# Optimization experiments

Measured on AMD Instinct MI355X. Metric: run time of the kernel, lower is better.

## Reference

```python
import jax, jax.numpy as jnp
import numpy as np

LN_EPS = 1e-5
FACTOR = 4

def layer_norm(x, w, b):
    mu = jnp.mean(x, axis=-1, keepdims=True)
    var = jnp.mean((x - mu) ** 2, axis=-1, keepdims=True)
    return (x - mu) * jax.lax.rsqrt(var + LN_EPS) * w + b

def setup_inputs() -> dict:
    key = jax.random.key(0)
    k1, k2, k3 = jax.random.split(key, 3)
    B, Sq, Skv, D = 4, 2048, 8192, 1024
    return {
        "query": jax.random.normal(k1, (B, Sq, D), dtype=jnp.float32),
        "key": jax.random.normal(k2, (B, Skv, D), dtype=jnp.float32),
        "value": jax.random.normal(k3, (B, Skv, D), dtype=jnp.float32),
        "ln_weight": jnp.ones((D,), dtype=jnp.float32),
        "ln_bias": jnp.zeros((D,), dtype=jnp.float32),
    }

def attention_downsampling(q, k, v, factor):
    # q: [B, S//f, D], k/v: [B, S, D]
    B, S, D = k.shape
    k_win = k.reshape(B, S // factor, factor, D)
    weights = jnp.einsum('bsd,bsfd->bsf', q, k_win).reshape(B, S)  # no softmax
    attn = weights[:, :, None] * v                                  # [B, S, D]
    attn = attn.reshape(B, S // factor, factor, D).sum(axis=2)      # [B, S//f, D]
    return attn

def reference(query, key, value, ln_weight, ln_bias):
    # pre-norm (post_norm=False): residual + attention over normed q/k/v
    qn = layer_norm(query, ln_weight, ln_bias)
    kn = layer_norm(key, ln_weight, ln_bias)
    vn = layer_norm(value, ln_weight, ln_bias)
    return query + attention_downsampling(qn, kn, vn, FACTOR)
```

## Files before the change

kernel.cpp:

```cpp
#include <hip/hip_runtime.h>


constexpr int D     = 1024;
constexpr int BLOCK = 256;
constexpr int NW    = BLOCK / 64;
constexpr float EPS = 1e-5f;

#define GLOBAL_AS const __attribute__((address_space(1))) void*
#define LDS_AS __attribute__((address_space(3))) void*

template<int CTRL>
__device__ __forceinline__ float dpp_add(float x) {
    int xi = __builtin_bit_cast(int, x);
    int yi = __builtin_amdgcn_update_dpp(0, xi, CTRL, 0xF, 0xF, true);
    return x + __builtin_bit_cast(float, yi);
}

__device__ __forceinline__ float wave_sum(float x) {
    x = dpp_add<0x111>(x);
    x = dpp_add<0x112>(x);
    x = dpp_add<0x114>(x);
    x = dpp_add<0x118>(x);
    x = dpp_add<0x142>(x);
    x = dpp_add<0x143>(x);
    return __builtin_bit_cast(float, __builtin_amdgcn_readlane(__builtin_bit_cast(int, x), 63));
}

template <int N>
__device__ __forceinline__ void block_reduce(float* vals, float* s_buf,
                                             int lane, int wid) {
#pragma unroll
    for (int i = 0; i < N; i++) {
        float x = wave_sum(vals[i]);
        if (lane == 0) s_buf[wid * N + i] = x;
    }
    __syncthreads();
#pragma unroll
    for (int i = 0; i < N; i++) {
        float t = 0.f;
#pragma unroll
        for (int w = 0; w < NW; w++) t += s_buf[w * N + i];
        vals[i] = t;
    }
    __syncthreads();
}

__global__ __launch_bounds__(BLOCK) void attn_ds_kernel(
    const float* __restrict__ q,
    const float* __restrict__ k,
    const float* __restrict__ v,
    const float* __restrict__ lw,
    const float* __restrict__ lb,
    float* __restrict__ out)
{
    __shared__ float kv_lds[8 * D];
    __shared__ float s_buf[NW * 18];

    const long row  = blockIdx.x;
    const int  tid  = threadIdx.x;
    const int  lane = tid & 63;
    const int  wid  = tid >> 6;
    const int  d0   = tid * 4;

    const float4 qv = *(const float4*)(q + row * D + d0);
    const float4 wv = *(const float4*)(lw + d0);
    const float4 bv = *(const float4*)(lb + d0);

    const float* kbase = k + row * (4L * D);
    const float* vbase = v + row * (4L * D);
#pragma unroll
    for (int i = 0; i < 8; i++) {
        const int c = wid + i * NW;
        const float* src = (c < 16 ? kbase : vbase) + (long)(c & 15) * 256 + lane * 4;
        float* dst = kv_lds + c * 256;
        __builtin_amdgcn_global_load_lds((GLOBAL_AS)src, (LDS_AS)dst, 16, 0, 0);
    }

    __syncthreads();

    float red[18];
    red[0] = qv.x + qv.y + qv.z + qv.w;
    red[1] = qv.x * qv.x + qv.y * qv.y + qv.z * qv.z + qv.w * qv.w;
    float4 kv4[4], vv4[4];
#pragma unroll
    for (int f = 0; f < 4; f++) {
        kv4[f] = *(const float4*)(kv_lds + f * D + d0);
        vv4[f] = *(const float4*)(kv_lds + (4 + f) * D + d0);
        red[2 + 2 * f]  = kv4[f].x + kv4[f].y + kv4[f].z + kv4[f].w;
        red[3 + 2 * f]  = kv4[f].x * kv4[f].x + kv4[f].y * kv4[f].y
                        + kv4[f].z * kv4[f].z + kv4[f].w * kv4[f].w;
        red[10 + 2 * f] = vv4[f].x + vv4[f].y + vv4[f].z + vv4[f].w;
        red[11 + 2 * f] = vv4[f].x * vv4[f].x + vv4[f].y * vv4[f].y
                        + vv4[f].z * vv4[f].z + vv4[f].w * vv4[f].w;
    }
    block_reduce<18>(red, s_buf, lane, wid);

    const float invD = 1.0f / (float)D;
    const float mu_q = red[0] * invD;
    const float rs_q = rsqrtf(fmaf(-mu_q, mu_q, red[1] * invD) + EPS);
    float mu_k[4], rs_k[4], mu_v[4], rs_v[4];
#pragma unroll
    for (int f = 0; f < 4; f++) {
        mu_k[f] = red[2 + 2 * f] * invD;
        rs_k[f] = rsqrtf(fmaf(-mu_k[f], mu_k[f], red[3 + 2 * f] * invD) + EPS);
        mu_v[f] = red[10 + 2 * f] * invD;
        rs_v[f] = rsqrtf(fmaf(-mu_v[f], mu_v[f], red[11 + 2 * f] * invD) + EPS);
    }

    float4 qn;
    qn.x = fmaf((qv.x - mu_q) * rs_q, wv.x, bv.x);
    qn.y = fmaf((qv.y - mu_q) * rs_q, wv.y, bv.y);
    qn.z = fmaf((qv.z - mu_q) * rs_q, wv.z, bv.z);
    qn.w = fmaf((qv.w - mu_q) * rs_q, wv.w, bv.w);
    float dp[4];
#pragma unroll
    for (int f = 0; f < 4; f++) {
        float4 kn;
        kn.x = fmaf((kv4[f].x - mu_k[f]) * rs_k[f], wv.x, bv.x);
        kn.y = fmaf((kv4[f].y - mu_k[f]) * rs_k[f], wv.y, bv.y);
        kn.z = fmaf((kv4[f].z - mu_k[f]) * rs_k[f], wv.z, bv.z);
        kn.w = fmaf((kv4[f].w - mu_k[f]) * rs_k[f], wv.w, bv.w);
        dp[f] = qn.x * kn.x + qn.y * kn.y + qn.z * kn.z + qn.w * kn.w;
    }
    block_reduce<4>(dp, s_buf, lane, wid);

    float4 acc = qv;
#pragma unroll
    for (int f = 0; f < 4; f++) {
        const float av = rs_v[f], cv = -mu_v[f] * rs_v[f], dpf = dp[f];
#define ACCO(m) { \
        float t  = fmaf(av, vv4[f].m, cv); \
        float vn = fmaf(t, wv.m, bv.m); \
        acc.m = fmaf(dpf, vn, acc.m); }
        ACCO(x) ACCO(y) ACCO(z) ACCO(w)
#undef ACCO
    }
    *(float4*)(out + row * D + d0) = acc;
}

extern "C" void kernel_launch(void* const* d_in, const int* in_sizes, int n_in,
                              void* d_out, int out_size, void* d_ws, size_t ws_size,
                              hipStream_t stream) {
    const float* q  = (const float*)d_in[0];
    const float* k  = (const float*)d_in[1];
    const float* v  = (const float*)d_in[2];
    const float* lw = (const float*)d_in[3];
    const float* lb = (const float*)d_in[4];
    float* out = (float*)d_out;

    const int rows = in_sizes[0] / D;
    attn_ds_kernel<<<dim3(rows), dim3(BLOCK), 0, stream>>>(q, k, v, lw, lb, out);
}
```

Baseline: 310.5 us.

## Process sixteen rows per block with double-buffered async LDS staging

Each block now handles sixteen consecutive rows, staging q, k and v for the next row into a second LDS buffer via global_load_lds while the current row is computed. Hand-placed vmcnt waits and raw barriers replace __syncthreads, and the trailing barrier of the last reduction is dropped. This is meant to overlap memory latency with compute and cut per-block launch overhead. In exchange it uses 72KB of LDS per block and launches far fewer blocks, which limits resident blocks per CU and may reduce the number of memory requests in flight.

```diff
diff --git a/kernel.cpp b/kernel.cpp
--- a/kernel.cpp
+++ b/kernel.cpp
@@ -4,6 +4,7 @@
 constexpr int D     = 1024;
 constexpr int BLOCK = 256;
 constexpr int NW    = BLOCK / 64;
+constexpr int NR    = 16;
 constexpr float EPS = 1e-5f;
 
 #define GLOBAL_AS const __attribute__((address_space(1))) void*
@@ -26,7 +27,13 @@
     return __builtin_bit_cast(float, __builtin_amdgcn_readlane(__builtin_bit_cast(int, x), 63));
 }
 
-template <int N>
+__device__ __forceinline__ void bar_lds() {
+    asm volatile("s_waitcnt lgkmcnt(0)" ::: "memory");
+    __builtin_amdgcn_s_barrier();
+    asm volatile("" ::: "memory");
+}
+
+template <int N, bool TRAIL>
 __device__ __forceinline__ void block_reduce(float* vals, float* s_buf,
                                              int lane, int wid) {
 #pragma unroll
@@ -34,7 +41,7 @@
         float x = wave_sum(vals[i]);
         if (lane == 0) s_buf[wid * N + i] = x;
     }
-    __syncthreads();
+    bar_lds();
 #pragma unroll
     for (int i = 0; i < N; i++) {
         float t = 0.f;
@@ -42,50 +49,43 @@
         for (int w = 0; w < NW; w++) t += s_buf[w * N + i];
         vals[i] = t;
     }
-    __syncthreads();
+    if (TRAIL) bar_lds();
 }
 
-__global__ __launch_bounds__(BLOCK) void attn_ds_kernel(
-    const float* __restrict__ q,
-    const float* __restrict__ k,
-    const float* __restrict__ v,
-    const float* __restrict__ lw,
-    const float* __restrict__ lb,
-    float* __restrict__ out)
-{
-    __shared__ float kv_lds[8 * D];
-    __shared__ float s_buf[NW * 18];
+__device__ __forceinline__ void stage_row(const float* __restrict__ q,
+                                          const float* __restrict__ k,
+                                          const float* __restrict__ v,
+                                          long row, float* buf, int wid, int lane) {
+    const int lo = lane * 4;
+    __builtin_amdgcn_global_load_lds((GLOBAL_AS)(q + row * D + wid * 256 + lo),
+                                     (LDS_AS)(buf + wid * 256), 16, 0, 0);
+    const float* kb = k + row * (4L * D) + wid * 256 + lo;
+    const float* vb = v + row * (4L * D) + wid * 256 + lo;
+    float* dk = buf + 1024 + wid * 256;
+    float* dv = buf + 5120 + wid * 256;
+#pragma unroll
+    for (int i = 0; i < 4; i++)
+        __builtin_amdgcn_global_load_lds((GLOBAL_AS)(kb + i * 1024),
+                                         (LDS_AS)(dk + i * 1024), 16, 0, 0);
+#pragma unroll
+    for (int i = 0; i < 4; i++)
+        __builtin_amdgcn_global_load_lds((GLOBAL_AS)(vb + i * 1024),
+                                         (LDS_AS)(dv + i * 1024), 16, 0, 0);
+}
 
-    const long row  = blockIdx.x;
-    const int  tid  = threadIdx.x;
-    const int  lane = tid & 63;
-    const int  wid  = tid >> 6;
-    const int  d0   = tid * 4;
-
-    const float4 qv = *(const float4*)(q + row * D + d0);
-    const float4 wv = *(const float4*)(lw + d0);
-    const float4 bv = *(const float4*)(lb + d0);
-
-    const float* kbase = k + row * (4L * D);
-    const float* vbase = v + row * (4L * D);
-#pragma unroll
-    for (int i = 0; i < 8; i++) {
-        const int c = wid + i * NW;
-        const float* src = (c < 16 ? kbase : vbase) + (long)(c & 15) * 256 + lane * 4;
-        float* dst = kv_lds + c * 256;
-        __builtin_amdgcn_global_load_lds((GLOBAL_AS)src, (LDS_AS)dst, 16, 0, 0);
-    }
-
-    __syncthreads();
-
+__device__ __forceinline__ void compute_row(const float* buf, float* s_buf,
+                                            const float4 wv, const float4 bv,
+                                            float* __restrict__ outp,
+                                            int lane, int wid, int d0) {
+    const float4 qv = *(const float4*)(buf + d0);
     float red[18];
     red[0] = qv.x + qv.y + qv.z + qv.w;
     red[1] = qv.x * qv.x + qv.y * qv.y + qv.z * qv.z + qv.w * qv.w;
     float4 kv4[4], vv4[4];
 #pragma unroll
     for (int f = 0; f < 4; f++) {
-        kv4[f] = *(const float4*)(kv_lds + f * D + d0);
-        vv4[f] = *(const float4*)(kv_lds + (4 + f) * D + d0);
+        kv4[f] = *(const float4*)(buf + 1024 + f * D + d0);
+        vv4[f] = *(const float4*)(buf + 5120 + f * D + d0);
         red[2 + 2 * f]  = kv4[f].x + kv4[f].y + kv4[f].z + kv4[f].w;
         red[3 + 2 * f]  = kv4[f].x * kv4[f].x + kv4[f].y * kv4[f].y
                         + kv4[f].z * kv4[f].z + kv4[f].w * kv4[f].w;
@@ -93,7 +93,7 @@
         red[11 + 2 * f] = vv4[f].x * vv4[f].x + vv4[f].y * vv4[f].y
                         + vv4[f].z * vv4[f].z + vv4[f].w * vv4[f].w;
     }
-    block_reduce<18>(red, s_buf, lane, wid);
+    block_reduce<18, true>(red, s_buf, lane, wid);
 
     const float invD = 1.0f / (float)D;
     const float mu_q = red[0] * invD;
@@ -122,7 +122,7 @@
         kn.w = fmaf((kv4[f].w - mu_k[f]) * rs_k[f], wv.w, bv.w);
         dp[f] = qn.x * kn.x + qn.y * kn.y + qn.z * kn.z + qn.w * kn.w;
     }
-    block_reduce<4>(dp, s_buf, lane, wid);
+    block_reduce<4, false>(dp, s_buf, lane, wid);
 
     float4 acc = qv;
 #pragma unroll
@@ -135,7 +135,52 @@
         ACCO(x) ACCO(y) ACCO(z) ACCO(w)
 #undef ACCO
     }
-    *(float4*)(out + row * D + d0) = acc;
+    *(float4*)(outp + d0) = acc;
+}
+
+__global__ __launch_bounds__(BLOCK, 2) void attn_ds_kernel(
+    const float* __restrict__ q,
+    const float* __restrict__ k,
+    const float* __restrict__ v,
+    const float* __restrict__ lw,
+    const float* __restrict__ lb,
+    float* __restrict__ out)
+{
+    __shared__ float buf0[9 * 1024];
+    __shared__ float buf1[9 * 1024];
+    __shared__ float s_buf[NW * 18];
+
+    const int tid  = threadIdx.x;
+    const int lane = tid & 63;
+    const int wid  = tid >> 6;
+    const int d0   = tid * 4;
+    const long r0  = (long)blockIdx.x * NR;
+
+    const float4 wv = *(const float4*)(lw + d0);
+    const float4 bv = *(const float4*)(lb + d0);
+    asm volatile("" :: "v"(wv.x), "v"(wv.y), "v"(wv.z), "v"(wv.w),
+                       "v"(bv.x), "v"(bv.y), "v"(bv.z), "v"(bv.w));
+
+    stage_row(q, k, v, r0, buf0, wid, lane);
+
+#pragma unroll 1
+    for (int i = 0; i < NR; i += 2) {
+        stage_row(q, k, v, r0 + i + 1, buf1, wid, lane);
+        asm volatile("s_waitcnt vmcnt(9)" ::: "memory");
+        __builtin_amdgcn_s_barrier();
+        asm volatile("" ::: "memory");
+        compute_row(buf0, s_buf, wv, bv, out + (r0 + i) * D, lane, wid, d0);
+
+        if (i + 2 < NR) {
+            stage_row(q, k, v, r0 + i + 2, buf0, wid, lane);
+            asm volatile("s_waitcnt vmcnt(9)" ::: "memory");
+        } else {
+            asm volatile("s_waitcnt vmcnt(0)" ::: "memory");
+        }
+        __builtin_amdgcn_s_barrier();
+        asm volatile("" ::: "memory");
+        compute_row(buf1, s_buf, wv, bv, out + (r0 + i + 1) * D, lane, wid, d0);
+    }
 }
 
 extern "C" void kernel_launch(void* const* d_in, const int* in_sizes, int n_in,
@@ -149,5 +194,6 @@
     float* out = (float*)d_out;
 
     const int rows = in_sizes[0] / D;
-    attn_ds_kernel<<<dim3(rows), dim3(BLOCK), 0, stream>>>(q, k, v, lw, lb, out);
+    const int grid = rows / NR;
+    attn_ds_kernel<<<dim3(grid), dim3(BLOCK), 0, stream>>>(q, k, v, lw, lb, out);
 }
```

After: 322.3 us. 3.8% more time.

## Process rows per wave with algebraic dot-product expansion, removing LDS and block syncs

Applied to the files above, without the earlier changes.

Each wavefront now handles whole rows (four rows per wave, looping), so every reduction becomes a wave-level DPP sum and LDS staging plus __syncthreads are dropped. The normalized q·k dot product is expanded algebraically into raw moment sums (Σq·k·w², Σq·w², Σk·w·b and so on), so the statistics and dot products can be reduced together in one pass. K loads are split into two halves to limit register pressure, and launch bounds request two blocks per CU. The cost is many more registers per thread and possible precision loss from the expanded formula.

```diff
diff --git a/kernel.cpp b/kernel.cpp
--- a/kernel.cpp
+++ b/kernel.cpp
@@ -1,13 +1,13 @@
 #include <hip/hip_runtime.h>
 
+
+typedef float f32x4 __attribute__((ext_vector_type(4)));
 
 constexpr int D     = 1024;
 constexpr int BLOCK = 256;
 constexpr int NW    = BLOCK / 64;
+constexpr int NRW   = 4;
 constexpr float EPS = 1e-5f;
-
-#define GLOBAL_AS const __attribute__((address_space(1))) void*
-#define LDS_AS __attribute__((address_space(3))) void*
 
 template<int CTRL>
 __device__ __forceinline__ float dpp_add(float x) {
@@ -26,116 +26,203 @@
     return __builtin_bit_cast(float, __builtin_amdgcn_readlane(__builtin_bit_cast(int, x), 63));
 }
 
-template <int N>
-__device__ __forceinline__ void block_reduce(float* vals, float* s_buf,
-                                             int lane, int wid) {
-#pragma unroll
-    for (int i = 0; i < N; i++) {
-        float x = wave_sum(vals[i]);
-        if (lane == 0) s_buf[wid * N + i] = x;
-    }
-    __syncthreads();
-#pragma unroll
-    for (int i = 0; i < N; i++) {
-        float t = 0.f;
-#pragma unroll
-        for (int w = 0; w < NW; w++) t += s_buf[w * N + i];
-        vals[i] = t;
-    }
-    __syncthreads();
-}
-
-__global__ __launch_bounds__(BLOCK) void attn_ds_kernel(
+__device__ __forceinline__ f32x4 vadd(f32x4 a, f32x4 b) {
+    f32x4 r;
+#pragma unroll
+    for (int j = 0; j < 4; j++) r[j] = a[j] + b[j];
+    return r;
+}
+__device__ __forceinline__ f32x4 vmul(f32x4 a, f32x4 b) {
+    f32x4 r;
+#pragma unroll
+    for (int j = 0; j < 4; j++) r[j] = a[j] * b[j];
+    return r;
+}
+__device__ __forceinline__ f32x4 vfma(f32x4 a, f32x4 b, f32x4 c) {
+    f32x4 r;
+#pragma unroll
+    for (int j = 0; j < 4; j++) r[j] = fmaf(a[j], b[j], c[j]);
+    return r;
+}
+__device__ __forceinline__ f32x4 vfma_ss(f32x4 a, float s, float c) {
+    f32x4 r;
+#pragma unroll
+    for (int j = 0; j < 4; j++) r[j] = fmaf(a[j], s, c);
+    return r;
+}
+__device__ __forceinline__ f32x4 vfma_sv(float s, f32x4 b, f32x4 c) {
+    f32x4 r;
+#pragma unroll
+    for (int j = 0; j < 4; j++) r[j] = fmaf(s, b[j], c[j]);
+    return r;
+}
+__device__ __forceinline__ float hsum(f32x4 a) { return (a[0] + a[1]) + (a[2] + a[3]); }
+
+__global__ __launch_bounds__(BLOCK, 2) void attn_ds_kernel(
     const float* __restrict__ q,
     const float* __restrict__ k,
     const float* __restrict__ v,
     const float* __restrict__ lw,
     const float* __restrict__ lb,
-    float* __restrict__ out)
+    float* __restrict__ out,
+    int rows)
 {
-    __shared__ float kv_lds[8 * D];
-    __shared__ float s_buf[NW * 18];
-
-    const long row  = blockIdx.x;
     const int  tid  = threadIdx.x;
     const int  lane = tid & 63;
     const int  wid  = tid >> 6;
-    const int  d0   = tid * 4;
-
-    const float4 qv = *(const float4*)(q + row * D + d0);
-    const float4 wv = *(const float4*)(lw + d0);
-    const float4 bv = *(const float4*)(lb + d0);
-
-    const float* kbase = k + row * (4L * D);
-    const float* vbase = v + row * (4L * D);
-#pragma unroll
-    for (int i = 0; i < 8; i++) {
-        const int c = wid + i * NW;
-        const float* src = (c < 16 ? kbase : vbase) + (long)(c & 15) * 256 + lane * 4;
-        float* dst = kv_lds + c * 256;
-        __builtin_amdgcn_global_load_lds((GLOBAL_AS)src, (LDS_AS)dst, 16, 0, 0);
+    const int  sl   = lane * 4;
+    const long gw   = (long)blockIdx.x * NW + wid;
+    long r = gw * NRW;
+
+    f32x4 wv[4], bv[4];
+#pragma unroll
+    for (int i = 0; i < 4; i++) {
+        wv[i] = *(const f32x4*)(lw + i * 256 + sl);
+        bv[i] = *(const f32x4*)(lb + i * 256 + sl);
     }
-
-    __syncthreads();
-
-    float red[18];
-    red[0] = qv.x + qv.y + qv.z + qv.w;
-    red[1] = qv.x * qv.x + qv.y * qv.y + qv.z * qv.z + qv.w * qv.w;
-    float4 kv4[4], vv4[4];
-#pragma unroll
-    for (int f = 0; f < 4; f++) {
-        kv4[f] = *(const float4*)(kv_lds + f * D + d0);
-        vv4[f] = *(const float4*)(kv_lds + (4 + f) * D + d0);
-        red[2 + 2 * f]  = kv4[f].x + kv4[f].y + kv4[f].z + kv4[f].w;
-        red[3 + 2 * f]  = kv4[f].x * kv4[f].x + kv4[f].y * kv4[f].y
-                        + kv4[f].z * kv4[f].z + kv4[f].w * kv4[f].w;
-        red[10 + 2 * f] = vv4[f].x + vv4[f].y + vv4[f].z + vv4[f].w;
-        red[11 + 2 * f] = vv4[f].x * vv4[f].x + vv4[f].y * vv4[f].y
-                        + vv4[f].z * vv4[f].z + vv4[f].w * vv4[f].w;
+    f32x4 aw2 = {0.f, 0.f, 0.f, 0.f}, awb = {0.f, 0.f, 0.f, 0.f}, ab2 = {0.f, 0.f, 0.f, 0.f};
+#pragma unroll
+    for (int i = 0; i < 4; i++) {
+        aw2 = vfma(wv[i], wv[i], aw2);
+        awb = vfma(wv[i], bv[i], awb);
+        ab2 = vfma(bv[i], bv[i], ab2);
     }
-    block_reduce<18>(red, s_buf, lane, wid);
-
+    const float Sw2 = wave_sum(hsum(aw2));
+    const float Swb = wave_sum(hsum(awb));
+    const float Sb2 = wave_sum(hsum(ab2));
     const float invD = 1.0f / (float)D;
-    const float mu_q = red[0] * invD;
-    const float rs_q = rsqrtf(fmaf(-mu_q, mu_q, red[1] * invD) + EPS);
-    float mu_k[4], rs_k[4], mu_v[4], rs_v[4];
-#pragma unroll
-    for (int f = 0; f < 4; f++) {
-        mu_k[f] = red[2 + 2 * f] * invD;
-        rs_k[f] = rsqrtf(fmaf(-mu_k[f], mu_k[f], red[3 + 2 * f] * invD) + EPS);
-        mu_v[f] = red[10 + 2 * f] * invD;
-        rs_v[f] = rsqrtf(fmaf(-mu_v[f], mu_v[f], red[11 + 2 * f] * invD) + EPS);
+
+#pragma unroll 1
+    for (int rr = 0; rr < NRW; rr++, r++) {
+        if (r >= rows) break;
+        const float* qp = q + r * (long)D;
+        const float* kp = k + r * (4L * D);
+        const float* vp = v + r * (4L * D);
+
+        f32x4 qv[4], vv[4][4], kw[2][4];
+#pragma unroll
+        for (int i = 0; i < 4; i++) qv[i] = *(const f32x4*)(qp + i * 256 + sl);
+#pragma unroll
+        for (int f = 0; f < 4; f++)
+#pragma unroll
+            for (int i = 0; i < 4; i++)
+                vv[f][i] = *(const f32x4*)(vp + f * D + i * 256 + sl);
+#pragma unroll
+        for (int h = 0; h < 2; h++)
+#pragma unroll
+            for (int i = 0; i < 4; i++)
+                kw[h][i] = *(const f32x4*)(kp + h * D + i * 256 + sl);
+
+        f32x4 a0 = {0.f,0.f,0.f,0.f}, a1 = a0, a2 = a0, a3 = a0;
+#pragma unroll
+        for (int i = 0; i < 4; i++) {
+            a0 = vadd(a0, qv[i]);
+            a1 = vfma(qv[i], qv[i], a1);
+            f32x4 t = vmul(qv[i], wv[i]);
+            a2 = vfma(t, wv[i], a2);
+            a3 = vfma(t, bv[i], a3);
+        }
+        float pSq = hsum(a0), pSqq = hsum(a1), pSqw2 = hsum(a2), pSqwb = hsum(a3);
+
+        float pSk[4], pSkk[4], pSkw2[4], pSkwb[4], pA[4];
+#pragma unroll
+        for (int f = 0; f < 2; f++) {
+            f32x4 s = {0.f,0.f,0.f,0.f}, ss = s, sw2a = s, swba = s, sA = s;
+#pragma unroll
+            for (int i = 0; i < 4; i++) {
+                f32x4 kk = kw[f][i];
+                s    = vadd(s, kk);
+                ss   = vfma(kk, kk, ss);
+                f32x4 t = vmul(kk, wv[i]);
+                sw2a = vfma(t, wv[i], sw2a);
+                swba = vfma(t, bv[i], swba);
+                f32x4 u = vmul(qv[i], wv[i]);
+                sA   = vfma(t, u, sA);
+            }
+            pSk[f] = hsum(s); pSkk[f] = hsum(ss);
+            pSkw2[f] = hsum(sw2a); pSkwb[f] = hsum(swba); pA[f] = hsum(sA);
+        }
+
+#pragma unroll
+        for (int h = 0; h < 2; h++)
+#pragma unroll
+            for (int i = 0; i < 4; i++)
+                kw[h][i] = *(const f32x4*)(kp + (2 + h) * D + i * 256 + sl);
+
+        float pSv[4], pSvv[4];
+#pragma unroll
+        for (int f = 0; f < 4; f++) {
+            f32x4 s = {0.f,0.f,0.f,0.f}, ss = s;
+#pragma unroll
+            for (int i = 0; i < 4; i++) {
+                s  = vadd(s, vv[f][i]);
+                ss = vfma(vv[f][i], vv[f][i], ss);
+            }
+            pSv[f] = hsum(s); pSvv[f] = hsum(ss);
+        }
+
+#pragma unroll
+        for (int f = 2; f < 4; f++) {
+            f32x4 s = {0.f,0.f,0.f,0.f}, ss = s, sw2a = s, swba = s, sA = s;
+#pragma unroll
+            for (int i = 0; i < 4; i++) {
+                f32x4 kk = kw[f - 2][i];
+                s    = vadd(s, kk);
+                ss   = vfma(kk, kk, ss);
+                f32x4 t = vmul(kk, wv[i]);
+                sw2a = vfma(t, wv[i], sw2a);
+                swba = vfma(t, bv[i], swba);
+                f32x4 u = vmul(qv[i], wv[i]);
+                sA   = vfma(t, u, sA);
+            }
+            pSk[f] = hsum(s); pSkk[f] = hsum(ss);
+            pSkw2[f] = hsum(sw2a); pSkwb[f] = hsum(swba); pA[f] = hsum(sA);
+        }
+
+        const float Sq   = wave_sum(pSq);
+        const float Sqq  = wave_sum(pSqq);
+        const float Sqw2 = wave_sum(pSqw2);
+        const float Sqwb = wave_sum(pSqwb);
+        float Sk[4], Skk[4], Skw2[4], Skwb[4], A[4], Sv[4], Svv[4];
+#pragma unroll
+        for (int f = 0; f < 4; f++) {
+            Sk[f]   = wave_sum(pSk[f]);
+            Skk[f]  = wave_sum(pSkk[f]);
+            Skw2[f] = wave_sum(pSkw2[f]);
+            Skwb[f] = wave_sum(pSkwb[f]);
+            A[f]    = wave_sum(pA[f]);
+            Sv[f]   = wave_sum(pSv[f]);
+            Svv[f]  = wave_sum(pSvv[f]);
+        }
+
+        const float mu_q = Sq * invD;
+        const float rs_q = rsqrtf(fmaf(-mu_q, mu_q, Sqq * invD) + EPS);
+        const float qlin = rs_q * (Sqwb - mu_q * Swb);
+        float dp[4], rs_v[4], cv[4];
+#pragma unroll
+        for (int f = 0; f < 4; f++) {
+            const float mu_k = Sk[f] * invD;
+            const float rs_k = rsqrtf(fmaf(-mu_k, mu_k, Skk[f] * invD) + EPS);
+            const float mu_v = Sv[f] * invD;
+            const float rv   = rsqrtf(fmaf(-mu_v, mu_v, Svv[f] * invD) + EPS);
+            const float cross = A[f] - mu_k * Sqw2 - mu_q * Skw2[f] + mu_q * mu_k * Sw2;
+            dp[f] = rs_q * rs_k * cross + qlin + rs_k * (Skwb[f] - mu_k * Swb) + Sb2;
+            rs_v[f] = rv;
+            cv[f]   = -mu_v * rv;
+        }
+
+#pragma unroll
+        for (int i = 0; i < 4; i++) {
+            f32x4 acc = qv[i];
+#pragma unroll
+            for (int f = 0; f < 4; f++) {
+                f32x4 t  = vfma_ss(vv[f][i], rs_v[f], cv[f]);
+                f32x4 vn = vfma(t, wv[i], bv[i]);
+                acc = vfma_sv(dp[f], vn, acc);
+            }
+            *(f32x4*)(out + r * (long)D + i * 256 + sl) = acc;
+        }
     }
-
-    float4 qn;
-    qn.x = fmaf((qv.x - mu_q) * rs_q, wv.x, bv.x);
-    qn.y = fmaf((qv.y - mu_q) * rs_q, wv.y, bv.y);
-    qn.z = fmaf((qv.z - mu_q) * rs_q, wv.z, bv.z);
-    qn.w = fmaf((qv.w - mu_q) * rs_q, wv.w, bv.w);
-    float dp[4];
-#pragma unroll
-    for (int f = 0; f < 4; f++) {
-        float4 kn;
-        kn.x = fmaf((kv4[f].x - mu_k[f]) * rs_k[f], wv.x, bv.x);
-        kn.y = fmaf((kv4[f].y - mu_k[f]) * rs_k[f], wv.y, bv.y);
-        kn.z = fmaf((kv4[f].z - mu_k[f]) * rs_k[f], wv.z, bv.z);
-        kn.w = fmaf((kv4[f].w - mu_k[f]) * rs_k[f], wv.w, bv.w);
-        dp[f] = qn.x * kn.x + qn.y * kn.y + qn.z * kn.z + qn.w * kn.w;
-    }
-    block_reduce<4>(dp, s_buf, lane, wid);
-
-    float4 acc = qv;
-#pragma unroll
-    for (int f = 0; f < 4; f++) {
-        const float av = rs_v[f], cv = -mu_v[f] * rs_v[f], dpf = dp[f];
-#define ACCO(m) { \
-        float t  = fmaf(av, vv4[f].m, cv); \
-        float vn = fmaf(t, wv.m, bv.m); \
-        acc.m = fmaf(dpf, vn, acc.m); }
-        ACCO(x) ACCO(y) ACCO(z) ACCO(w)
-#undef ACCO
-    }
-    *(float4*)(out + row * D + d0) = acc;
 }
 
 extern "C" void kernel_launch(void* const* d_in, const int* in_sizes, int n_in,
@@ -149,5 +236,6 @@
     float* out = (float*)d_out;
 
     const int rows = in_sizes[0] / D;
-    attn_ds_kernel<<<dim3(rows), dim3(BLOCK), 0, stream>>>(q, k, v, lw, lb, out);
-}
+    const int grid = (rows + NW * NRW - 1) / (NW * NRW);
+    attn_ds_kernel<<<dim3(grid), dim3(BLOCK), 0, stream>>>(q, k, v, lw, lb, out, rows);
+}
```

Measured after the change: 312.6 us. Within noise of the previous version (+0.7%).
